# Kernel optimization log

Measured on AMD Instinct MI355X. Metric: run time of the kernel, lower is better.

The kernel has to match this reference:

```python
import jax, jax.numpy as jnp
import numpy as np

CUBE_NEIGHBOR = jnp.array([[-1, 0, 0], [0, -1, 0], [0, 0, -1]], dtype=jnp.int64)


def setup_inputs() -> dict:
    key = jax.random.key(0)
    ks = jax.random.split(key, 6)
    k, F, H, O = 128, 64, 128, 2
    N_es = 200000
    topo_feat = jax.random.normal(ks[0], (k, k, k, F), dtype=jnp.float32)
    esid = jax.random.randint(ks[1], (N_es, 3), 0, k).astype(jnp.int64)
    W1 = jax.random.normal(ks[2], (2 * F, H), dtype=jnp.float32) * (1.0 / np.sqrt(2 * F))
    b1 = jnp.zeros((H,), dtype=jnp.float32)
    W2 = jax.random.normal(ks[3], (H, H), dtype=jnp.float32) * (1.0 / np.sqrt(H))
    b2 = jnp.zeros((H,), dtype=jnp.float32)
    W3 = jax.random.normal(ks[4], (H, O), dtype=jnp.float32) * (1.0 / np.sqrt(H))
    b3 = jnp.zeros((O,), dtype=jnp.float32)
    return {"topo_feat": topo_feat, "esid": esid, "W1": W1, "b1": b1,
            "W2": W2, "b2": b2, "W3": W3, "b3": b3, "k": k}


def reference(topo_feat, esid, W1, b1, W2, b2, W3, b3, k):
    N_es = esid.shape[0]
    F = topo_feat.shape[-1]
    # gather edge features: [N_es, F]
    edge_feat = topo_feat[esid[:, 0], esid[:, 1], esid[:, 2]]
    # clamped neighbor indices: [N_es, 3, 3]
    eid_nn = jnp.clip(esid[:, None, :] + CUBE_NEIGHBOR, 0, k - 1)
    # gather neighbor features: [N_es, 3, F]
    feat_nn = topo_feat[eid_nn[..., 0], eid_nn[..., 1], eid_nn[..., 2]]
    # CubeFaceNet: repeat edge feat across the 3 faces, concat -> [N_es, 3, 2F]
    feat = jnp.concatenate(
        [jnp.broadcast_to(edge_feat[:, None, :], (N_es, 3, F)), feat_nn], axis=-1)
    # MLP forward_simple: dense + ReLU stack
    h = jax.nn.relu(feat @ W1 + b1)
    h = jax.nn.relu(h @ W2 + b2)
    out_face = h @ W3 + b3                     # [N_es, 3, 2]
    out_face = jnp.swapaxes(out_face, 1, 2)    # [N_es, 2, 3]
    # predict_type == 'Softmax' -> softmax over class dim (dim=1)
    return jax.nn.softmax(out_face, axis=1)
```

## Files before the change

### kernel.cpp

```cpp
#include <hip/hip_runtime.h>

typedef __attribute__((ext_vector_type(8))) short s16x8;
typedef __attribute__((ext_vector_type(16))) float f32x16;

#define THREADS 512
#define WAVES 8
#define TROWS 32
#define RPB (WAVES * TROWS)

__device__ __forceinline__ short f2bf(float f) {
    unsigned u = __float_as_uint(f);
    u += 0x7fffu + ((u >> 16) & 1u);
    return (short)(u >> 16);
}

__device__ __forceinline__ unsigned cvt_pk(float lo, float hi) {
    unsigned r;
    asm("v_cvt_pk_bf16_f32 %0, %1, %2" : "=v"(r) : "v"(lo), "v"(hi));
    return r;
}

__device__ __forceinline__ int swz(int row, int col) {
    return row * 128 + ((((col >> 3) ^ (row & 15)) << 3) | (col & 7));
}

template <int S>
__device__ __forceinline__ float dpp_ror(float v) {
    int x = __builtin_amdgcn_update_dpp(0, __float_as_int(v), 0x120 | S, 0xf, 0xf, false);
    return __int_as_float(x);
}

__device__ __forceinline__ float red16(float v) {
    v += dpp_ror<1>(v);
    v += dpp_ror<2>(v);
    v += dpp_ror<4>(v);
    v += dpp_ror<8>(v);
    return v;
}

__device__ __forceinline__ s16x8 pack8(float4 a, float4 b) {
    union { unsigned u[4]; s16x8 v; } z;
    z.u[0] = cvt_pk(a.x, a.y); z.u[1] = cvt_pk(a.z, a.w);
    z.u[2] = cvt_pk(b.x, b.y); z.u[3] = cvt_pk(b.z, b.w);
    return z.v;
}

__launch_bounds__(THREADS, 2)
__global__ void edgeface_kernel(
    const float* __restrict__ topo, const int* __restrict__ esid,
    const float* __restrict__ W1, const float* __restrict__ b1,
    const float* __restrict__ W2, const float* __restrict__ b2,
    const float* __restrict__ W3, const float* __restrict__ b3,
    float* __restrict__ out, int nRows, int kg)
{
    __shared__ __align__(16) short sW1[128 * 128];
    __shared__ __align__(16) short sW2[128 * 128];
    __shared__ __align__(16) short sT[WAVES * TROWS * 128];

    const int tid = threadIdx.x;

    for (int idx = tid; idx < 128 * 128; idx += THREADS) {
        int kk = idx >> 7, n = idx & 127;
        int d = swz(n, kk);
        sW1[d] = f2bf(W1[idx]);
        sW2[d] = f2bf(W2[idx]);
    }
    __syncthreads();

    const int w = tid >> 6, lane = tid & 63;
    short* tile = sT + w * (TROWS * 128);
    const int c31 = lane & 31;
    const int h   = lane >> 5;

    float rb1[4], rb2[4], w3d[4];
    #pragma unroll
    for (int n = 0; n < 4; ++n) {
        int col = n * 32 + c31;
        rb1[n] = b1[col];
        rb2[n] = b2[col];
        w3d[n] = W3[col * 2 + 1] - W3[col * 2 + 0];
    }
    const float b3d = b3[1] - b3[0];

    const int G = gridDim.x;
    const int nTiles = (nRows + RPB - 1) / RPB;

    int e0, e1, e2;
    {
        int R = min(blockIdx.x * RPB + w * TROWS + c31, nRows - 1);
        int n = R / 3;
        e0 = esid[n * 3 + 0]; e1 = esid[n * 3 + 1]; e2 = esid[n * 3 + 2];
    }

    float4 pf[16];
    {
        int R = min(blockIdx.x * RPB + w * TROWS + c31, nRows - 1);
        int f = R - 3 * (R / 3);
        long ea = (((long)e0 * kg + e1) * kg + e2) * 64;
        long na = ((((long)((f == 0) ? max(e0 - 1, 0) : e0)) * kg
                  + ((f == 1) ? max(e1 - 1, 0) : e1)) * kg
                  + ((f == 2) ? max(e2 - 1, 0) : e2)) * 64;
        const float4* pe = (const float4*)(topo + ea);
        const float4* pn = (const float4*)(topo + na);
        #pragma unroll
        for (int ks = 0; ks < 4; ++ks) {
            pf[2 * ks + 0] = pe[ks * 4 + h * 2 + 0];
            pf[2 * ks + 1] = pe[ks * 4 + h * 2 + 1];
            pf[8 + 2 * ks + 0] = pn[ks * 4 + h * 2 + 0];
            pf[8 + 2 * ks + 1] = pn[ks * 4 + h * 2 + 1];
        }
        int Rn = min((blockIdx.x + G) * RPB + w * TROWS + c31, nRows - 1);
        int nn = Rn / 3;
        e0 = esid[nn * 3 + 0]; e1 = esid[nn * 3 + 1]; e2 = esid[nn * 3 + 2];
    }

    for (int tI = blockIdx.x; tI < nTiles; tI += G) {
        const int base = tI * RPB + w * TROWS;

        s16x8 a[8];
        #pragma unroll
        for (int ks = 0; ks < 4; ++ks) {
            a[ks]     = pack8(pf[2 * ks], pf[2 * ks + 1]);
            a[4 + ks] = pack8(pf[8 + 2 * ks], pf[8 + 2 * ks + 1]);
        }

        {
            int Rn = min((tI + G) * RPB + w * TROWS + c31, nRows - 1);
            int f = Rn - 3 * (Rn / 3);
            long ea = (((long)e0 * kg + e1) * kg + e2) * 64;
            long na = ((((long)((f == 0) ? max(e0 - 1, 0) : e0)) * kg
                      + ((f == 1) ? max(e1 - 1, 0) : e1)) * kg
                      + ((f == 2) ? max(e2 - 1, 0) : e2)) * 64;
            const float4* pe = (const float4*)(topo + ea);
            const float4* pn = (const float4*)(topo + na);
            #pragma unroll
            for (int ks = 0; ks < 4; ++ks) {
                pf[2 * ks + 0] = pe[ks * 4 + h * 2 + 0];
                pf[2 * ks + 1] = pe[ks * 4 + h * 2 + 1];
                pf[8 + 2 * ks + 0] = pn[ks * 4 + h * 2 + 0];
                pf[8 + 2 * ks + 1] = pn[ks * 4 + h * 2 + 1];
            }
        }
        {
            int Rn = min((tI + 2 * G) * RPB + w * TROWS + c31, nRows - 1);
            int nn = Rn / 3;
            e0 = esid[nn * 3 + 0]; e1 = esid[nn * 3 + 1]; e2 = esid[nn * 3 + 2];
        }

        #pragma unroll
        for (int n = 0; n < 4; ++n) {
            f32x16 c = {0.f,0.f,0.f,0.f,0.f,0.f,0.f,0.f,0.f,0.f,0.f,0.f,0.f,0.f,0.f,0.f};
            #pragma unroll
            for (int ks = 0; ks < 8; ++ks) {
                s16x8 bf = *(const s16x8*)(sW1 + swz(n * 32 + c31, ks * 16 + h * 8));
                c = __builtin_amdgcn_mfma_f32_32x32x16_bf16(a[ks], bf, c, 0, 0, 0);
            }
            int col = n * 32 + c31;
            #pragma unroll
            for (int rg = 0; rg < 8; ++rg) {
                float h0 = fmaxf(c[2 * rg + 0] + rb1[n], 0.f);
                float h1 = fmaxf(c[2 * rg + 1] + rb1[n], 0.f);
                unsigned pk = cvt_pk(h0, h1);
                int r0 = ((2 * rg) & 3) + 8 * ((2 * rg) >> 2) + 4 * h;
                tile[swz(r0 + 0, col)] = (short)pk;
                tile[swz(r0 + 1, col)] = (short)(pk >> 16);
            }
        }

        #pragma unroll
        for (int ks = 0; ks < 8; ++ks)
            a[ks] = *(const s16x8*)(tile + swz(c31, ks * 16 + h * 8));

        float pd[16];
        #pragma unroll
        for (int i = 0; i < 16; ++i) pd[i] = 0.f;
        #pragma unroll
        for (int n = 0; n < 4; ++n) {
            f32x16 c = {0.f,0.f,0.f,0.f,0.f,0.f,0.f,0.f,0.f,0.f,0.f,0.f,0.f,0.f,0.f,0.f};
            #pragma unroll
            for (int ks = 0; ks < 8; ++ks) {
                s16x8 bf = *(const s16x8*)(sW2 + swz(n * 32 + c31, ks * 16 + h * 8));
                c = __builtin_amdgcn_mfma_f32_32x32x16_bf16(a[ks], bf, c, 0, 0, 0);
            }
            #pragma unroll
            for (int reg = 0; reg < 16; ++reg) {
                float hh = fmaxf(c[reg] + rb2[n], 0.f);
                pd[reg] = fmaf(hh, w3d[n], pd[reg]);
            }
        }

        float dsel = 0.f;
        #pragma unroll
        for (int reg = 0; reg < 16; ++reg) {
            float v = red16(pd[reg]);
            v += __int_as_float(__builtin_amdgcn_ds_swizzle(__float_as_int(v), 0x401F));
            if ((c31 >> 1) == reg) dsel = v;
        }

        {
            int o  = c31 & 1;
            int rg = c31 >> 1;
            int row = (rg & 3) + 8 * (rg >> 2) + 4 * h;
            float d = dsel + b3d;
            float p = 1.f / (1.f + __expf(o ? -d : d));
            int Ro = base + row;
            if (Ro < nRows) {
                int n = Ro / 3, ff = Ro - 3 * n;
                out[n * 6 + o * 3 + ff] = p;
            }
        }
    }
}

extern "C" void kernel_launch(void* const* d_in, const int* in_sizes, int n_in,
                              void* d_out, int out_size, void* d_ws, size_t ws_size,
                              hipStream_t stream) {
    const float* topo = (const float*)d_in[0];
    const int*   esid = (const int*)d_in[1];
    const float* W1 = (const float*)d_in[2];
    const float* b1 = (const float*)d_in[3];
    const float* W2 = (const float*)d_in[4];
    const float* b2 = (const float*)d_in[5];
    const float* W3 = (const float*)d_in[6];
    const float* b3 = (const float*)d_in[7];
    float* out = (float*)d_out;

    int nRows = in_sizes[1];
    int H = in_sizes[3];
    int F = (in_sizes[2] / H) / 2;
    long vol = (long)in_sizes[0] / F;
    int kg = 1;
    while ((long)(kg + 1) * (kg + 1) * (kg + 1) <= vol) ++kg;

    if (nRows <= 0) return;
    edgeface_kernel<<<dim3(256), dim3(THREADS), 0, stream>>>(
        topo, esid, W1, b1, W2, b2, W3, b3, out, nRows, kg);
}
```

Baseline: 63.34 us.

## Keep MLP activations in registers via transposed MFMA chain and fold biases

Swaps the MFMA operand roles so weights are the A operand and features the B operand. Each layer's output then lands in registers in the layout the next layer needs as its B operand, which removes the per-wave LDS staging tile and its write/read round trip. Biases are folded into an extra K block through an augmented ones vector, and W2/W3 rows are permuted to match the register layout. The final projection becomes a small MFMA instead of DPP reductions. This adds extra MFMAs for the bias block and a padded W3 tile, and keeps more packed activations live in registers.

```diff
diff --git a/kernel.cpp b/kernel.cpp
--- a/kernel.cpp
+++ b/kernel.cpp
@@ -4,9 +4,9 @@
 typedef __attribute__((ext_vector_type(16))) float f32x16;
 
 #define THREADS 512
-#define WAVES 8
 #define TROWS 32
-#define RPB (WAVES * TROWS)
+#define RPB (8 * TROWS)
+#define WS 152
 
 __device__ __forceinline__ short f2bf(float f) {
     unsigned u = __float_as_uint(f);
@@ -20,22 +20,15 @@
     return r;
 }
 
-__device__ __forceinline__ int swz(int row, int col) {
-    return row * 128 + ((((col >> 3) ^ (row & 15)) << 3) | (col & 7));
-}
-
-template <int S>
-__device__ __forceinline__ float dpp_ror(float v) {
-    int x = __builtin_amdgcn_update_dpp(0, __float_as_int(v), 0x120 | S, 0xf, 0xf, false);
-    return __int_as_float(x);
-}
-
-__device__ __forceinline__ float red16(float v) {
-    v += dpp_ror<1>(v);
-    v += dpp_ror<2>(v);
-    v += dpp_ror<4>(v);
-    v += dpp_ror<8>(v);
-    return v;
+__device__ __forceinline__ int kperm(int k) {
+    int j = ((k >> 4) & 1) * 4 + ((k >> 1) & 3);
+    return (k >> 5) * 32 + (j >> 1) * 8 + (j & 1) * 2 + ((k >> 3) & 1) * 4 + (k & 1);
+}
+
+__device__ __forceinline__ int wswz(int c, int k) {
+    int g = k >> 3;
+    int gs = (g < 16) ? (g ^ ((c >> 3) & 15)) : g;
+    return c * WS + gs * 8 + (k & 7);
 }
 
 __device__ __forceinline__ s16x8 pack8(float4 a, float4 b) {
@@ -53,34 +46,43 @@
     const float* __restrict__ W3, const float* __restrict__ b3,
     float* __restrict__ out, int nRows, int kg)
 {
-    __shared__ __align__(16) short sW1[128 * 128];
-    __shared__ __align__(16) short sW2[128 * 128];
-    __shared__ __align__(16) short sT[WAVES * TROWS * 128];
+    __shared__ __align__(16) short sW1t[128 * WS];
+    __shared__ __align__(16) short sW2t[128 * WS];
+    __shared__ __align__(16) short sW3t[32 * WS];
 
     const int tid = threadIdx.x;
 
-    for (int idx = tid; idx < 128 * 128; idx += THREADS) {
-        int kk = idx >> 7, n = idx & 127;
-        int d = swz(n, kk);
-        sW1[d] = f2bf(W1[idx]);
-        sW2[d] = f2bf(W2[idx]);
+    for (int e = tid; e < 128 * WS; e += THREADS) {
+        int c = e & 127, kk = e >> 7;
+        float v1 = (kk < 128) ? W1[kk * 128 + c] : ((kk == 128) ? b1[c] : 0.f);
+        float v2 = (kk < 128) ? W2[kperm(kk) * 128 + c] : ((kk == 128) ? b2[c] : 0.f);
+        int d = wswz(c, kk);
+        sW1t[d] = f2bf(v1);
+        sW2t[d] = f2bf(v2);
+    }
+    for (int e = tid; e < 32 * WS; e += THREADS) {
+        int c = e & 31, kk = e >> 5;
+        float v = 0.f;
+        if (c == 0) {
+            if (kk < 128) {
+                int p = kperm(kk);
+                v = W3[p * 2 + 1] - W3[p * 2 + 0];
+            } else if (kk == 128) {
+                v = b3[1] - b3[0];
+            }
+        }
+        sW3t[wswz(c, kk)] = f2bf(v);
     }
     __syncthreads();
 
     const int w = tid >> 6, lane = tid & 63;
-    short* tile = sT + w * (TROWS * 128);
     const int c31 = lane & 31;
     const int h   = lane >> 5;
 
-    float rb1[4], rb2[4], w3d[4];
-    #pragma unroll
-    for (int n = 0; n < 4; ++n) {
-        int col = n * 32 + c31;
-        rb1[n] = b1[col];
-        rb2[n] = b2[col];
-        w3d[n] = W3[col * 2 + 1] - W3[col * 2 + 0];
-    }
-    const float b3d = b3[1] - b3[0];
+    union { unsigned u[4]; s16x8 v; } za;
+    za.u[0] = (h == 0) ? 0x00003F80u : 0u;
+    za.u[1] = 0u; za.u[2] = 0u; za.u[3] = 0u;
+    const s16x8 bfaug = za.v;
 
     const int G = gridDim.x;
     const int nTiles = (nRows + RPB - 1) / RPB;
@@ -117,11 +119,11 @@
     for (int tI = blockIdx.x; tI < nTiles; tI += G) {
         const int base = tI * RPB + w * TROWS;
 
-        s16x8 a[8];
+        s16x8 bf[8];
         #pragma unroll
         for (int ks = 0; ks < 4; ++ks) {
-            a[ks]     = pack8(pf[2 * ks], pf[2 * ks + 1]);
-            a[4 + ks] = pack8(pf[8 + 2 * ks], pf[8 + 2 * ks + 1]);
+            bf[ks]     = pack8(pf[2 * ks], pf[2 * ks + 1]);
+            bf[4 + ks] = pack8(pf[8 + 2 * ks], pf[8 + 2 * ks + 1]);
         }
 
         {
@@ -147,67 +149,70 @@
             e0 = esid[nn * 3 + 0]; e1 = esid[nn * 3 + 1]; e2 = esid[nn * 3 + 2];
         }
 
+        unsigned pk[4][8];
         #pragma unroll
         for (int n = 0; n < 4; ++n) {
             f32x16 c = {0.f,0.f,0.f,0.f,0.f,0.f,0.f,0.f,0.f,0.f,0.f,0.f,0.f,0.f,0.f,0.f};
             #pragma unroll
             for (int ks = 0; ks < 8; ++ks) {
-                s16x8 bf = *(const s16x8*)(sW1 + swz(n * 32 + c31, ks * 16 + h * 8));
-                c = __builtin_amdgcn_mfma_f32_32x32x16_bf16(a[ks], bf, c, 0, 0, 0);
-            }
-            int col = n * 32 + c31;
-            #pragma unroll
-            for (int rg = 0; rg < 8; ++rg) {
-                float h0 = fmaxf(c[2 * rg + 0] + rb1[n], 0.f);
-                float h1 = fmaxf(c[2 * rg + 1] + rb1[n], 0.f);
-                unsigned pk = cvt_pk(h0, h1);
-                int r0 = ((2 * rg) & 3) + 8 * ((2 * rg) >> 2) + 4 * h;
-                tile[swz(r0 + 0, col)] = (short)pk;
-                tile[swz(r0 + 1, col)] = (short)(pk >> 16);
-            }
-        }
-
-        #pragma unroll
-        for (int ks = 0; ks < 8; ++ks)
-            a[ks] = *(const s16x8*)(tile + swz(c31, ks * 16 + h * 8));
-
-        float pd[16];
-        #pragma unroll
-        for (int i = 0; i < 16; ++i) pd[i] = 0.f;
-        #pragma unroll
-        for (int n = 0; n < 4; ++n) {
+                s16x8 af = *(const s16x8*)(sW1t + wswz(n * 32 + c31, ks * 16 + h * 8));
+                c = __builtin_amdgcn_mfma_f32_32x32x16_bf16(af, bf[ks], c, 0, 0, 0);
+            }
+            {
+                s16x8 af = *(const s16x8*)(sW1t + wswz(n * 32 + c31, 128 + h * 8));
+                c = __builtin_amdgcn_mfma_f32_32x32x16_bf16(af, bfaug, c, 0, 0, 0);
+            }
+            #pragma unroll
+            for (int j = 0; j < 8; ++j)
+                pk[n][j] = cvt_pk(fmaxf(c[2 * j + 0], 0.f), fmaxf(c[2 * j + 1], 0.f));
+        }
+
+        unsigned pk2[4][8];
+        #pragma unroll
+        for (int n2 = 0; n2 < 4; ++n2) {
             f32x16 c = {0.f,0.f,0.f,0.f,0.f,0.f,0.f,0.f,0.f,0.f,0.f,0.f,0.f,0.f,0.f,0.f};
             #pragma unroll
             for (int ks = 0; ks < 8; ++ks) {
-                s16x8 bf = *(const s16x8*)(sW2 + swz(n * 32 + c31, ks * 16 + h * 8));
-                c = __builtin_amdgcn_mfma_f32_32x32x16_bf16(a[ks], bf, c, 0, 0, 0);
-            }
-            #pragma unroll
-            for (int reg = 0; reg < 16; ++reg) {
-                float hh = fmaxf(c[reg] + rb2[n], 0.f);
-                pd[reg] = fmaf(hh, w3d[n], pd[reg]);
-            }
-        }
-
-        float dsel = 0.f;
-        #pragma unroll
-        for (int reg = 0; reg < 16; ++reg) {
-            float v = red16(pd[reg]);
-            v += __int_as_float(__builtin_amdgcn_ds_swizzle(__float_as_int(v), 0x401F));
-            if ((c31 >> 1) == reg) dsel = v;
-        }
-
+                s16x8 af = *(const s16x8*)(sW2t + wswz(n2 * 32 + c31, ks * 16 + h * 8));
+                union { unsigned u[4]; s16x8 v; } bb;
+                bb.u[0] = pk[ks >> 1][(ks & 1) * 4 + 0];
+                bb.u[1] = pk[ks >> 1][(ks & 1) * 4 + 1];
+                bb.u[2] = pk[ks >> 1][(ks & 1) * 4 + 2];
+                bb.u[3] = pk[ks >> 1][(ks & 1) * 4 + 3];
+                c = __builtin_amdgcn_mfma_f32_32x32x16_bf16(af, bb.v, c, 0, 0, 0);
+            }
+            {
+                s16x8 af = *(const s16x8*)(sW2t + wswz(n2 * 32 + c31, 128 + h * 8));
+                c = __builtin_amdgcn_mfma_f32_32x32x16_bf16(af, bfaug, c, 0, 0, 0);
+            }
+            #pragma unroll
+            for (int j = 0; j < 8; ++j)
+                pk2[n2][j] = cvt_pk(fmaxf(c[2 * j + 0], 0.f), fmaxf(c[2 * j + 1], 0.f));
+        }
+
+        f32x16 c3 = {0.f,0.f,0.f,0.f,0.f,0.f,0.f,0.f,0.f,0.f,0.f,0.f,0.f,0.f,0.f,0.f};
+        #pragma unroll
+        for (int ks = 0; ks < 8; ++ks) {
+            s16x8 af = *(const s16x8*)(sW3t + wswz(c31, ks * 16 + h * 8));
+            union { unsigned u[4]; s16x8 v; } bb;
+            bb.u[0] = pk2[ks >> 1][(ks & 1) * 4 + 0];
+            bb.u[1] = pk2[ks >> 1][(ks & 1) * 4 + 1];
+            bb.u[2] = pk2[ks >> 1][(ks & 1) * 4 + 2];
+            bb.u[3] = pk2[ks >> 1][(ks & 1) * 4 + 3];
+            c3 = __builtin_amdgcn_mfma_f32_32x32x16_bf16(af, bb.v, c3, 0, 0, 0);
+        }
         {
-            int o  = c31 & 1;
-            int rg = c31 >> 1;
-            int row = (rg & 3) + 8 * (rg >> 2) + 4 * h;
-            float d = dsel + b3d;
-            float p = 1.f / (1.f + __expf(o ? -d : d));
-            int Ro = base + row;
-            if (Ro < nRows) {
-                int n = Ro / 3, ff = Ro - 3 * n;
-                out[n * 6 + o * 3 + ff] = p;
-            }
+            s16x8 af = *(const s16x8*)(sW3t + wswz(c31, 128 + h * 8));
+            c3 = __builtin_amdgcn_mfma_f32_32x32x16_bf16(af, bfaug, c3, 0, 0, 0);
+        }
+
+        float sel = c3[0];
+        float dd = sel + __shfl_xor(sel, 32, 64);
+        float p = 1.f / (1.f + __expf(h ? -dd : dd));
+        int R = base + c31;
+        if (R < nRows) {
+            int n = R / 3, ff = R - 3 * n;
+            out[n * 6 + h * 3 + ff] = p;
         }
     }
 }
```

Measured after the change: 75.17 us. 1.19x slower.
